# Performance work log

Measured on AMD Instinct MI355X. Metric: run time of the kernel, lower is better.

## Reference

```python
import jax, jax.numpy as jnp
import numpy as np

E = 256      # embedding_dim
H = 16       # head_num
D = 16       # qkv_dim
FF = 512     # ff_hidden_dim
L = 5        # encoder_layer_num
B = 4        # batch
N = 256      # node_cnt
EPS = 1e-5   # InstanceNorm eps


def setup_inputs() -> dict:
    key = jax.random.key(0)
    ks = jax.random.split(key, 16)
    s = 0.05

    def nrm(k, shape):
        return jax.random.normal(k, shape, dtype=jnp.float32) * s

    return {
        "data": jax.random.normal(ks[0], (B, N, N), dtype=jnp.float32),
        "node_rand": jax.random.uniform(ks[1], (B, N, 1), dtype=jnp.float32),
        # Cross_Encoder input projections (Linear(1, E))
        "Wnode": nrm(ks[2], (1, E)), "bnode": jnp.zeros((E,), jnp.float32),
        "Wedge": nrm(ks[3], (1, E)), "bedge": jnp.zeros((E,), jnp.float32),
        # Per layer (L) x per block (2: row/col) weights
        "Wq": nrm(ks[4], (L, 2, E, H * D)),
        "Wk": nrm(ks[5], (L, 2, E, H * D)),
        "Wv": nrm(ks[6], (L, 2, E, H * D)),
        "Wcomb": nrm(ks[7], (L, 2, H * D, E)),
        "bcomb": jnp.zeros((L, 2, E), jnp.float32),
        "n1w": jnp.ones((L, 2, E), jnp.float32),
        "n1b": jnp.zeros((L, 2, E), jnp.float32),
        "W1": nrm(ks[8], (L, 2, E, FF)),
        "b1": jnp.zeros((L, 2, FF), jnp.float32),
        "W2": nrm(ks[9], (L, 2, FF, E)),
        "b2": jnp.zeros((L, 2, E), jnp.float32),
        "n2w": jnp.ones((L, 2, E), jnp.float32),
        "n2b": jnp.zeros((L, 2, E), jnp.float32),
        # MixedScore edge-bias projection per block: E -> H channels
        "Wmix": nrm(ks[10], (L, 2, E, H)),
    }


def _instance_norm(x, w, b):
    # x: [B, N, E]; InstanceNorm1d after transpose -> normalize over node dim N per (B, channel)
    mu = jnp.mean(x, axis=1, keepdims=True)
    var = jnp.var(x, axis=1, keepdims=True)
    return (x - mu) * jax.lax.rsqrt(var + EPS) * w + b


def reference(data, node_rand, Wnode, bnode, Wedge, bedge,
              Wq, Wk, Wv, Wcomb, bcomb, n1w, n1b,
              W1, b1, W2, b2, n2w, n2b, Wmix):
    inv_sqrt_d = jnp.float32(1.0) / jnp.sqrt(jnp.float32(D))

    def block(row, col, edge, i, j):
        # row, col: [B, N, E]; edge: [B, N, N, E]
        q = (row @ Wq[i, j]).reshape(B, N, H, D)
        k = (col @ Wk[i, j]).reshape(B, N, H, D)
        v = (col @ Wv[i, j]).reshape(B, N, H, D)
        score = jnp.einsum('bnhd,bmhd->bhnm', q, k) * inv_sqrt_d
        score = score + jnp.einsum('bnme,eh->bhnm', edge, Wmix[i, j])
        w = jax.nn.softmax(score, axis=-1)
        out = jnp.einsum('bhnm,bmhd->bnhd', w, v).reshape(B, N, H * D)
        mh = out @ Wcomb[i, j] + bcomb[i, j]
        o1 = _instance_norm(row + mh, n1w[i, j], n1b[i, j])
        ff = jax.nn.relu(o1 @ W1[i, j] + b1[i, j]) @ W2[i, j] + b2[i, j]
        return _instance_norm(o1 + ff, n2w[i, j], n2b[i, j])

    # compute_normalized_matrices: per-batch global min-max scaling
    flat = data.reshape(B, -1)
    mn = flat.min(axis=1).reshape(B, 1, 1)
    mx = flat.max(axis=1).reshape(B, 1, 1)
    rng = mx - mn
    rng = jnp.where(rng == 0, jnp.float32(1.0), rng)
    scaled = (data - mn) / rng

    edge = scaled[..., None] @ Wedge + bedge           # [B, N, N, E]
    emb = node_rand @ Wnode + bnode                    # [B, N, E]

    row, col = emb, emb
    for i in range(L):
        row_new = block(row, col, edge, i, 0)
        col = block(col, row, jnp.swapaxes(edge, 1, 2), i, 1)
        row = row_new
    return row, col
```

## Files before the change

kernel.cpp:

```cpp
#include <hip/hip_runtime.h>
#include <hip/hip_bf16.h>

#define E 256
#define H 16
#define DD 16
#define FFH 512
#define LAYERS 5
#define BB 4
#define NN 256
#define MROWS 1024

typedef __attribute__((ext_vector_type(8))) short bfrag;
typedef __attribute__((ext_vector_type(4))) float f32x4;
typedef __attribute__((ext_vector_type(8))) unsigned short us8;
typedef unsigned short u16;

__device__ __forceinline__ void bsplit(float v, u16& h, u16& l) {
    unsigned u = __float_as_uint(v);
    u16 hh = (u16)((u + 0x7fffu + ((u >> 16) & 1u)) >> 16);
    float r = v - __uint_as_float((unsigned)hh << 16);
    unsigned u2 = __float_as_uint(r);
    h = hh;
    l = (u16)((u2 + 0x7fffu + ((u2 >> 16) & 1u)) >> 16);
}

union PrepS {
    float tile[32 * 33];
    struct { u16 th[64 * 40], tl[64 * 40]; } wp;
    struct { float smin[4], smax[4]; } mm;
};

__global__ __launch_bounds__(256) void k_prep(
    const float* __restrict__ data, const float* __restrict__ node_rand,
    const float* __restrict__ Wnode, const float* __restrict__ bnode,
    const float* __restrict__ Wedge, const float* __restrict__ bedge,
    const float* __restrict__ Wmix,
    const float* __restrict__ Wq, const float* __restrict__ Wk, const float* __restrict__ Wv,
    const float* __restrict__ Wc, const float* __restrict__ W1, const float* __restrict__ W2,
    float* __restrict__ pmin, float* __restrict__ pmax, float* __restrict__ c1c0,
    float* __restrict__ rowb, float* __restrict__ colb,
    u16* rowh, u16* rowl, u16* colh, u16* coll,
    float* __restrict__ dataT,
    u16* qh, u16* ql, u16* kh, u16* kl_, u16* vh, u16* vl,
    u16* ch, u16* cl, u16* f1h, u16* f1l, u16* f2h, u16* f2l) {
    __shared__ PrepS ps;
    int bid = blockIdx.x;
    int t = threadIdx.x;
    if (bid < 64) {
        int b = bid >> 4, p = bid & 15;
        const float* src = data + (size_t)b * NN * NN + p * 4096;
        float lmin = 1e30f, lmax = -1e30f;
        #pragma unroll
        for (int i = 0; i < 16; i++) {
            float v = src[t + i * 256];
            lmin = fminf(lmin, v);
            lmax = fmaxf(lmax, v);
        }
        #pragma unroll
        for (int off = 32; off; off >>= 1) {
            lmin = fminf(lmin, __shfl_down(lmin, off));
            lmax = fmaxf(lmax, __shfl_down(lmax, off));
        }
        int wid = t >> 6, lane = t & 63;
        if (lane == 0) { ps.mm.smin[wid] = lmin; ps.mm.smax[wid] = lmax; }
        __syncthreads();
        if (t == 0) {
            pmin[b * 16 + p] = fminf(fminf(ps.mm.smin[0], ps.mm.smin[1]), fminf(ps.mm.smin[2], ps.mm.smin[3]));
            pmax[b * 16 + p] = fmaxf(fmaxf(ps.mm.smax[0], ps.mm.smax[1]), fmaxf(ps.mm.smax[2], ps.mm.smax[3]));
        }
    } else if (bid < 1088) {
        int idx = (bid - 64) * 256 + t;
        int bn = idx >> 8, e = idx & 255;
        float v = node_rand[bn] * Wnode[e] + bnode[e];
        rowb[idx] = v;
        colb[idx] = v;
        u16 h, l;
        bsplit(v, h, l);
        rowh[idx] = h; rowl[idx] = l;
        colh[idx] = h; coll[idx] = l;
    } else if (bid < 1344) {
        int local = bid - 1088;
        int bx = local & 7, by = (local >> 3) & 7, b = local >> 6;
        int r0 = by * 32, c0 = bx * 32;
        int tx = t & 31, ty = t >> 5;
        const float* src = data + (size_t)b * NN * NN;
        float* dst = dataT + (size_t)b * NN * NN;
        #pragma unroll
        for (int i = 0; i < 4; i++)
            ps.tile[(ty + 8 * i) * 33 + tx] = src[(size_t)(r0 + ty + 8 * i) * NN + c0 + tx];
        __syncthreads();
        #pragma unroll
        for (int i = 0; i < 4; i++)
            dst[(size_t)(c0 + ty + 8 * i) * NN + r0 + tx] = ps.tile[tx * 33 + ty + 8 * i];
    } else if (bid < 3904) {
        int id = bid - 1344;
        const float* W; u16 *Dh, *Dl; int K, N, mat, s, nt;
        if (id < 1280) {
            int seg = id / 320, local = id % 320;
            mat = local >> 5; int rem = local & 31; s = rem >> 2; nt = rem & 3;
            K = 256; N = 256;
            W  = seg == 0 ? Wq : seg == 1 ? Wk : seg == 2 ? Wv : Wc;
            Dh = seg == 0 ? qh : seg == 1 ? kh : seg == 2 ? vh : ch;
            Dl = seg == 0 ? ql : seg == 1 ? kl_ : seg == 2 ? vl : cl;
        } else if (id < 1920) {
            int local = id - 1280;
            mat = local >> 6; int rem = local & 63; s = rem >> 3; nt = rem & 7;
            K = 256; N = 512; W = W1; Dh = f1h; Dl = f1l;
        } else {
            int local = id - 1920;
            mat = local >> 6; int rem = local & 63; s = rem >> 2; nt = rem & 3;
            K = 512; N = 256; W = W2; Dh = f2h; Dl = f2l;
        }
        int kk = t >> 3, nl = (t & 7) * 8;
        const float* p = W + (size_t)mat * K * N + (size_t)(s * 32 + kk) * N + nt * 64 + nl;
        float4 f0 = *(const float4*)p;
        float4 f1v = *(const float4*)(p + 4);
        float fv[8] = {f0.x, f0.y, f0.z, f0.w, f1v.x, f1v.y, f1v.z, f1v.w};
        #pragma unroll
        for (int i = 0; i < 8; i++) bsplit(fv[i], ps.wp.th[(nl + i) * 40 + kk], ps.wp.tl[(nl + i) * 40 + kk]);
        __syncthreads();
        int n = t >> 2, ko = (t & 3) * 8;
        size_t dbase = (size_t)mat * K * N + (size_t)s * N * 32 + (size_t)nt * 64 * 32
                     + (size_t)n * 32 + ko;
        *(us8*)(Dh + dbase) = *(const us8*)&ps.wp.th[n * 40 + ko];
        *(us8*)(Dl + dbase) = *(const us8*)&ps.wp.tl[n * 40 + ko];
    } else {
        if (t < LAYERS * 2 * H) {
            int lj = t >> 4, h = t & 15;
            float c1 = 0.f, c0 = 0.f;
            for (int e = 0; e < E; e++) {
                float wm = Wmix[(lj * E + e) * H + h];
                c1 += Wedge[e] * wm;
                c0 += bedge[e] * wm;
            }
            c1c0[t] = c1;
            c1c0[160 + t] = c0;
        }
    }
}

__device__ __forceinline__ void mfma_gemm(const u16* __restrict__ Ah, const u16* __restrict__ Al,
                                          const u16* __restrict__ Bh, const u16* __restrict__ Bl,
                                          const float* __restrict__ bias, const float* __restrict__ R,
                                          float* __restrict__ Cf, u16* __restrict__ Ch,
                                          u16* __restrict__ Cl, int K, int Ncols, int relu) {
    __shared__ u16 AsH[32 * 136], AsL[32 * 136], BsH[64 * 136], BsL[64 * 136];
    int t = threadIdx.x;
    int lane = t & 63, wave = t >> 6;
    int quad = lane >> 4, l16 = lane & 15;
    int wy = wave >> 1, wx = wave & 1;
    int mBase = blockIdx.x * 32, nBase = blockIdx.y * 64;
    f32x4 acc0 = {0.f, 0.f, 0.f, 0.f}, acc1 = acc0;
    int arow = t >> 3, ak = (t & 7) * 16;
    int bcol = lane, bq = wave;
    const int nslab = K >> 7;
    const u16* apH = Ah + (size_t)(mBase + arow) * K + ak;
    const u16* apL = Al + (size_t)(mBase + arow) * K + ak;
    const size_t sstr = (size_t)Ncols * 32;
    size_t bbase = (size_t)bq * sstr + (size_t)(nBase + bcol) * 32;
    const u16* bpH = Bh + bbase;
    const u16* bpL = Bl + bbase;
    us8 rah0 = *(const us8*)apH, rah1 = *(const us8*)(apH + 8);
    us8 ral0 = *(const us8*)apL, ral1 = *(const us8*)(apL + 8);
    us8 rbh0 = *(const us8*)(bpH + 0);
    us8 rbh1 = *(const us8*)(bpH + 8);
    us8 rbh2 = *(const us8*)(bpH + 16);
    us8 rbh3 = *(const us8*)(bpH + 24);
    us8 rbl0 = *(const us8*)(bpL + 0);
    us8 rbl1 = *(const us8*)(bpL + 8);
    us8 rbl2 = *(const us8*)(bpL + 16);
    us8 rbl3 = *(const us8*)(bpL + 24);
    for (int s = 0; s < nslab; s++) {
        __syncthreads();
        *(us8*)&AsH[arow * 136 + ak] = rah0;  *(us8*)&AsH[arow * 136 + ak + 8] = rah1;
        *(us8*)&AsL[arow * 136 + ak] = ral0;  *(us8*)&AsL[arow * 136 + ak + 8] = ral1;
        {
            int bb = bcol * 136 + bq * 32;
            *(us8*)&BsH[bb + 0] = rbh0;  *(us8*)&BsH[bb + 8] = rbh1;
            *(us8*)&BsH[bb + 16] = rbh2; *(us8*)&BsH[bb + 24] = rbh3;
            *(us8*)&BsL[bb + 0] = rbl0;  *(us8*)&BsL[bb + 8] = rbl1;
            *(us8*)&BsL[bb + 16] = rbl2; *(us8*)&BsL[bb + 24] = rbl3;
        }
        __syncthreads();
        if (s + 1 < nslab) {
            rah0 = *(const us8*)(apH + (s + 1) * 128);
            rah1 = *(const us8*)(apH + (s + 1) * 128 + 8);
            ral0 = *(const us8*)(apL + (s + 1) * 128);
            ral1 = *(const us8*)(apL + (s + 1) * 128 + 8);
            const u16* nbH = bpH + (size_t)(4 * (s + 1)) * sstr;
            const u16* nbL = bpL + (size_t)(4 * (s + 1)) * sstr;
            rbh0 = *(const us8*)(nbH + 0);  rbh1 = *(const us8*)(nbH + 8);
            rbh2 = *(const us8*)(nbH + 16); rbh3 = *(const us8*)(nbH + 24);
            rbl0 = *(const us8*)(nbL + 0);  rbl1 = *(const us8*)(nbL + 8);
            rbl2 = *(const us8*)(nbL + 16); rbl3 = *(const us8*)(nbL + 24);
        }
        #pragma unroll
        for (int c = 0; c < 4; c++) {
            bfrag a_h = *(const bfrag*)&AsH[(wy * 16 + l16) * 136 + c * 32 + quad * 8];
            bfrag a_l = *(const bfrag*)&AsL[(wy * 16 + l16) * 136 + c * 32 + quad * 8];
            bfrag b_h0 = *(const bfrag*)&BsH[(wx * 32 + l16) * 136 + c * 32 + quad * 8];
            bfrag b_h1 = *(const bfrag*)&BsH[(wx * 32 + 16 + l16) * 136 + c * 32 + quad * 8];
            bfrag b_l0 = *(const bfrag*)&BsL[(wx * 32 + l16) * 136 + c * 32 + quad * 8];
            bfrag b_l1 = *(const bfrag*)&BsL[(wx * 32 + 16 + l16) * 136 + c * 32 + quad * 8];
            acc0 = __builtin_amdgcn_mfma_f32_16x16x32_bf16(a_h, b_h0, acc0, 0, 0, 0);
            acc1 = __builtin_amdgcn_mfma_f32_16x16x32_bf16(a_h, b_h1, acc1, 0, 0, 0);
            acc0 = __builtin_amdgcn_mfma_f32_16x16x32_bf16(a_h, b_l0, acc0, 0, 0, 0);
            acc1 = __builtin_amdgcn_mfma_f32_16x16x32_bf16(a_h, b_l1, acc1, 0, 0, 0);
            acc0 = __builtin_amdgcn_mfma_f32_16x16x32_bf16(a_l, b_h0, acc0, 0, 0, 0);
            acc1 = __builtin_amdgcn_mfma_f32_16x16x32_bf16(a_l, b_h1, acc1, 0, 0, 0);
        }
    }
    int col0 = nBase + wx * 32 + l16;
    int col1 = col0 + 16;
    float bia0 = bias ? bias[col0] : 0.f;
    float bia1 = bias ? bias[col1] : 0.f;
    #pragma unroll
    for (int r = 0; r < 4; r++) {
        int row0 = mBase + wy * 16 + quad * 4 + r;
        float v0 = acc0[r] + bia0, v1 = acc1[r] + bia1;
        if (R) {
            v0 += R[(size_t)row0 * Ncols + col0];
            v1 += R[(size_t)row0 * Ncols + col1];
        }
        if (relu) {
            v0 = fmaxf(v0, 0.f); v1 = fmaxf(v1, 0.f);
        }
        if (Cf) {
            Cf[(size_t)row0 * Ncols + col0] = v0;
            Cf[(size_t)row0 * Ncols + col1] = v1;
        } else {
            u16 h, l;
            bsplit(v0, h, l); Ch[(size_t)row0 * Ncols + col0] = h; Cl[(size_t)row0 * Ncols + col0] = l;
            bsplit(v1, h, l); Ch[(size_t)row0 * Ncols + col1] = h; Cl[(size_t)row0 * Ncols + col1] = l;
        }
    }
}

__global__ __launch_bounds__(256) void k_qkv(const u16* __restrict__ rowh, const u16* __restrict__ rowl,
                                             const u16* __restrict__ colh, const u16* __restrict__ coll,
                                             const u16* __restrict__ WqTh, const u16* __restrict__ WqTl,
                                             const u16* __restrict__ WkTh, const u16* __restrict__ WkTl,
                                             const u16* __restrict__ WvTh, const u16* __restrict__ WvTl,
                                             int lb2,
                                             float* q0, float* k0, float* v0,
                                             float* q1, float* k1, float* v1) {
    int z = blockIdx.z;
    int j = z / 3, w = z % 3;
    const u16* Ah = (w == 0) ? (j ? colh : rowh) : (j ? rowh : colh);
    const u16* Al = (w == 0) ? (j ? coll : rowl) : (j ? rowl : coll);
    const u16* Wh = (w == 0 ? WqTh : (w == 1 ? WkTh : WvTh)) + (size_t)(lb2 + j) * E * E;
    const u16* Wl = (w == 0 ? WqTl : (w == 1 ? WkTl : WvTl)) + (size_t)(lb2 + j) * E * E;
    float* outs[6] = {q0, k0, v0, q1, k1, v1};
    mfma_gemm(Ah, Al, Wh, Wl, nullptr, nullptr, outs[z], nullptr, nullptr, E, E, 0);
}

__global__ __launch_bounds__(256) void k_mgemm(const u16* Ah0, const u16* Al0,
                                               const u16* Ah1, const u16* Al1,
                                               const u16* __restrict__ Bh, const u16* __restrict__ Bl,
                                               int lb2, long wstride,
                                               const float* __restrict__ biasl, int bstride,
                                               const float* R0, const float* R1,
                                               float* Cf0, float* Cf1,
                                               u16* Ch0, u16* Cl0, u16* Ch1, u16* Cl1,
                                               int K, int Ncols, int relu) {
    int j = blockIdx.z;
    mfma_gemm(j ? Ah1 : Ah0, j ? Al1 : Al0,
              Bh + (size_t)(lb2 + j) * wstride, Bl + (size_t)(lb2 + j) * wstride,
              biasl ? biasl + (size_t)j * bstride : nullptr,
              R0 ? (j ? R1 : R0) : nullptr,
              Cf0 ? (j ? Cf1 : Cf0) : nullptr,
              Ch0 ? (j ? Ch1 : Ch0) : nullptr,
              Cl0 ? (j ? Cl1 : Cl0) : nullptr,
              K, Ncols, relu);
}

__global__ __launch_bounds__(256) void k_attn(const float* __restrict__ q0, const float* __restrict__ k0,
                                              const float* __restrict__ v0, const float* __restrict__ q1,
                                              const float* __restrict__ k1, const float* __restrict__ v1,
                                              const float* __restrict__ data, const float* __restrict__ dataT,
                                              const float* __restrict__ pmin, const float* __restrict__ pmax,
                                              const float* __restrict__ c1c0, int lj_base,
                                              u16* __restrict__ atth0, u16* __restrict__ attl0,
                                              u16* __restrict__ atth1, u16* __restrict__ attl1) {
    int wgid = blockIdx.x;
    int r8 = wgid & 7;
    int qd = wgid >> 3;
    int ng = qd & 7;
    int bhj = r8 * 16 + (qd >> 3);
    int bh = bhj >> 1;
    int j = bhj & 1;
    int b = bh >> 4, h = bh & 15;
    const float* q = j ? q1 : q0;
    const float* k = j ? k1 : k0;
    const float* v = j ? v1 : v0;
    float mn = 1e30f, mx = -1e30f;
    #pragma unroll
    for (int p = 0; p < 16; p++) {
        mn = fminf(mn, pmin[b * 16 + p]);
        mx = fmaxf(mx, pmax[b * 16 + p]);
    }
    float rng = mx - mn;
    if (rng == 0.f) rng = 1.f;
    float inv = 1.f / rng;
    float c1 = c1c0[(lj_base + j) * 16 + h];
    float c0 = c1c0[160 + (lj_base + j) * 16 + h];
    float c1p = inv * c1;
    float c0p = c0 - mn * c1p;

    __shared__ float kl[256 * 20];
    __shared__ float vl[256 * 20];
    int t = threadIdx.x;
    int lane = t & 63, w = t >> 6;
    int r = lane >> 3, ml = lane & 7;
    int n = ng * 32 + w * 8 + r;

    float qr[16];
    const float* qp = q + ((size_t)(b * NN + n) * E) + h * DD;
    #pragma unroll
    for (int d4 = 0; d4 < 4; d4++) {
        float4 q4 = *(const float4*)(qp + d4 * 4);
        qr[d4 * 4 + 0] = q4.x; qr[d4 * 4 + 1] = q4.y;
        qr[d4 * 4 + 2] = q4.z; qr[d4 * 4 + 3] = q4.w;
    }

    {
        int c = t & 3, mb = t >> 2;
        #pragma unroll
        for (int it = 0; it < 4; it++) {
            int m = mb + 64 * it;
            const float* kp = k + ((size_t)(b * NN + m) * E) + h * DD + c * 4;
            const float* vp = v + ((size_t)(b * NN + m) * E) + h * DD + c * 4;
            *(float4*)&kl[m * 20 + c * 4] = *(const float4*)kp;
            *(float4*)&vl[m * 20 + c * 4] = *(const float4*)vp;
        }
    }
    __syncthreads();

    const float* pedge = (j ? dataT : data) + (size_t)b * NN * NN + (size_t)n * NN;

    float sum = 0.f;
    float acc[16] = {};
    for (int i = 0; i < 32; i++) {
        int m = ml + 8 * i;
        float4 ka = *(const float4*)&kl[m * 20 + 0];
        float4 kb = *(const float4*)&kl[m * 20 + 4];
        float4 kc = *(const float4*)&kl[m * 20 + 8];
        float4 kd = *(const float4*)&kl[m * 20 + 12];
        float s0 = qr[0] * ka.x + qr[1] * ka.y + qr[2] * ka.z + qr[3] * ka.w;
        float s1 = qr[4] * kb.x + qr[5] * kb.y + qr[6] * kb.z + qr[7] * kb.w;
        float s2 = qr[8] * kc.x + qr[9] * kc.y + qr[10] * kc.z + qr[11] * kc.w;
        float s3 = qr[12] * kd.x + qr[13] * kd.y + qr[14] * kd.z + qr[15] * kd.w;
        float s = ((s0 + s1) + (s2 + s3)) * 0.25f + pedge[m] * c1p + c0p;
        float e = __expf(s);
        sum += e;
        float4 va = *(const float4*)&vl[m * 20 + 0];
        float4 vb = *(const float4*)&vl[m * 20 + 4];
        float4 vc = *(const float4*)&vl[m * 20 + 8];
        float4 vd = *(const float4*)&vl[m * 20 + 12];
        acc[0] += e * va.x;  acc[1] += e * va.y;  acc[2] += e * va.z;  acc[3] += e * va.w;
        acc[4] += e * vb.x;  acc[5] += e * vb.y;  acc[6] += e * vb.z;  acc[7] += e * vb.w;
        acc[8] += e * vc.x;  acc[9] += e * vc.y;  acc[10] += e * vc.z; acc[11] += e * vc.w;
        acc[12] += e * vd.x; acc[13] += e * vd.y; acc[14] += e * vd.z; acc[15] += e * vd.w;
    }
    #pragma unroll
    for (int mask = 1; mask <= 4; mask <<= 1) {
        sum += __shfl_xor(sum, mask);
        #pragma unroll
        for (int d = 0; d < 16; d++) acc[d] += __shfl_xor(acc[d], mask);
    }
    if (ml == 0) {
        float invs = 1.f / sum;
        u16 hh[16], ll[16];
        #pragma unroll
        for (int d = 0; d < 16; d++) bsplit(acc[d] * invs, hh[d], ll[d]);
        size_t base = ((size_t)(b * NN + n) * E) + h * DD;
        u16* oh = (j ? atth1 : atth0) + base;
        u16* ol = (j ? attl1 : attl0) + base;
        *(us8*)oh = *(const us8*)&hh[0];
        *(us8*)(oh + 8) = *(const us8*)&hh[8];
        *(us8*)ol = *(const us8*)&ll[0];
        *(us8*)(ol + 8) = *(const us8*)&ll[8];
    }
}

__global__ __launch_bounds__(256) void k_inorm(const float* __restrict__ Y0, const float* __restrict__ Y1,
                                               const float* __restrict__ wl, const float* __restrict__ bl,
                                               int pstride,
                                               float* Of0, float* Of1,
                                               u16* Oh0, u16* Ol0, u16* Oh1, u16* Ol1,
                                               float* __restrict__ fout) {
    int b = blockIdx.x, j = blockIdx.y;
    int ec = blockIdx.z * 8;
    const float* Y = (j ? Y1 : Y0) + (size_t)b * NN * E;
    float* O = (j ? Of1 : Of0) + (size_t)b * NN * E;
    u16* Oh = (j ? Oh1 : Oh0) + (size_t)b * NN * E;
    u16* Ol = (j ? Ol1 : Ol0) + (size_t)b * NN * E;
    const float* w = wl + (size_t)j * pstride;
    const float* bb = bl + (size_t)j * pstride;
    int t = threadIdx.x;
    int et = t & 7, n0 = t >> 3;
    int e = ec + et;
    float vals[8];
    float s = 0.f, s2 = 0.f;
    #pragma unroll
    for (int kk = 0; kk < 8; kk++) {
        float v = Y[(size_t)(n0 + 32 * kk) * E + e];
        vals[kk] = v;
        s += v;
        s2 += v * v;
    }
    __shared__ float ps[32 * 9], ps2[32 * 9];
    ps[n0 * 9 + et] = s;
    ps2[n0 * 9 + et] = s2;
    __syncthreads();
    float st = 0.f, st2 = 0.f;
    #pragma unroll
    for (int kk = 0; kk < 32; kk++) { st += ps[kk * 9 + et]; st2 += ps2[kk * 9 + et]; }
    float mu = st * (1.f / NN);
    float var = fmaxf(st2 * (1.f / NN) - mu * mu, 0.f);
    float scale = w[e] * rsqrtf(var + 1e-5f);
    float shift = bb[e] - mu * scale;
    #pragma unroll
    for (int kk = 0; kk < 8; kk++) {
        float vv = vals[kk] * scale + shift;
        size_t idx = (size_t)(n0 + 32 * kk) * E + e;
        O[idx] = vv;
        u16 hh, ll;
        bsplit(vv, hh, ll);
        Oh[idx] = hh;
        Ol[idx] = ll;
        if (fout) fout[(size_t)j * (BB * NN * E) + (size_t)b * NN * E + idx] = vv;
    }
}


extern "C" void kernel_launch(void* const* d_in, const int* in_sizes, int n_in,
                              void* d_out, int out_size, void* d_ws, size_t ws_size,
                              hipStream_t stream) {
    const float* data      = (const float*)d_in[0];
    const float* node_rand = (const float*)d_in[1];
    const float* Wnode     = (const float*)d_in[2];
    const float* bnode     = (const float*)d_in[3];
    const float* Wedge     = (const float*)d_in[4];
    const float* bedge     = (const float*)d_in[5];
    const float* Wq        = (const float*)d_in[6];
    const float* Wk        = (const float*)d_in[7];
    const float* Wv        = (const float*)d_in[8];
    const float* Wcomb     = (const float*)d_in[9];
    const float* bcomb     = (const float*)d_in[10];
    const float* n1w       = (const float*)d_in[11];
    const float* n1b       = (const float*)d_in[12];
    const float* W1        = (const float*)d_in[13];
    const float* b1        = (const float*)d_in[14];
    const float* W2        = (const float*)d_in[15];
    const float* b2        = (const float*)d_in[16];
    const float* n2w       = (const float*)d_in[17];
    const float* n2b       = (const float*)d_in[18];
    const float* Wmix      = (const float*)d_in[19];
    float* out = (float*)d_out;

    float* ws = (float*)d_ws;
    const size_t T = (size_t)MROWS * E;
    const size_t TF = (size_t)MROWS * FFH;
    float* dataT = ws + 0 * T;
    float* row   = ws + 1 * T;
    float* col   = ws + 2 * T;
    float* q0    = ws + 3 * T;
    float* q1    = ws + 4 * T;
    float* k0    = ws + 5 * T;
    float* k1    = ws + 6 * T;
    float* v0    = ws + 7 * T;
    float* v1    = ws + 8 * T;
    float* o1f0  = ws + 9 * T;
    float* o1f1  = ws + 10 * T;
    float* pmin  = ws + 11 * T;
    float* pmax  = pmin + 64;
    float* c1c0  = pmax + 64;
    u16* us = (u16*)(ws + 11 * T + 512);
    auto nxt = [&](size_t n) { u16* p = us; us += n; return p; };
    u16* rowh = nxt(T);  u16* rowl = nxt(T);
    u16* colh = nxt(T);  u16* coll = nxt(T);
    u16* atth0 = nxt(T); u16* attl0 = nxt(T);
    u16* atth1 = nxt(T); u16* attl1 = nxt(T);
    u16* o1h0 = nxt(T);  u16* o1l0 = nxt(T);
    u16* o1h1 = nxt(T);  u16* o1l1 = nxt(T);
    u16* ffhh0 = nxt(TF); u16* ffhl0 = nxt(TF);
    u16* ffhh1 = nxt(TF); u16* ffhl1 = nxt(TF);
    const size_t EE10 = (size_t)10 * E * E;
    const size_t EF10 = (size_t)10 * E * FFH;
    u16* WqTh = nxt(EE10); u16* WqTl = nxt(EE10);
    u16* WkTh = nxt(EE10); u16* WkTl = nxt(EE10);
    u16* WvTh = nxt(EE10); u16* WvTl = nxt(EE10);
    u16* WcTh = nxt(EE10); u16* WcTl = nxt(EE10);
    u16* W1Th = nxt(EF10); u16* W1Tl = nxt(EF10);
    u16* W2Th = nxt(EF10); u16* W2Tl = nxt(EF10);
    float* y0 = q0;   float* y1 = q1;
    float* y20 = q0;  float* y21 = q1;

    k_prep<<<3905, 256, 0, stream>>>(data, node_rand, Wnode, bnode,
                                     Wedge, bedge, Wmix,
                                     Wq, Wk, Wv, Wcomb, W1, W2,
                                     pmin, pmax, c1c0,
                                     row, col, rowh, rowl, colh, coll, dataT,
                                     WqTh, WqTl, WkTh, WkTl, WvTh, WvTl,
                                     WcTh, WcTl, W1Th, W1Tl, W2Th, W2Tl);

    for (int l = 0; l < LAYERS; l++) {
        int lb2 = l * 2;
        k_qkv<<<dim3(32, 4, 6), 256, 0, stream>>>(rowh, rowl, colh, coll,
                                                  WqTh, WqTl, WkTh, WkTl, WvTh, WvTl, lb2,
                                                  q0, k0, v0, q1, k1, v1);
        k_attn<<<dim3(1024), 256, 0, stream>>>(q0, k0, v0, q1, k1, v1, data, dataT,
                                               pmin, pmax, c1c0, lb2,
                                               atth0, attl0, atth1, attl1);
        k_mgemm<<<dim3(32, 4, 2), 256, 0, stream>>>(atth0, attl0, atth1, attl1,
                                                    WcTh, WcTl, lb2, (long)E * E,
                                                    bcomb, E,
                                                    row, col, y0, y1,
                                                    nullptr, nullptr, nullptr, nullptr,
                                                    E, E, 0);
        k_inorm<<<dim3(BB, 2, 32), 256, 0, stream>>>(y0, y1,
                                                     n1w + (size_t)lb2 * E, n1b + (size_t)lb2 * E, E,
                                                     o1f0, o1f1, o1h0, o1l0, o1h1, o1l1, nullptr);
        k_mgemm<<<dim3(32, 8, 2), 256, 0, stream>>>(o1h0, o1l0, o1h1, o1l1,
                                                    W1Th, W1Tl, lb2, (long)E * FFH,
                                                    b1, FFH,
                                                    nullptr, nullptr, nullptr, nullptr,
                                                    ffhh0, ffhl0, ffhh1, ffhl1,
                                                    E, FFH, 1);
        k_mgemm<<<dim3(32, 4, 2), 256, 0, stream>>>(ffhh0, ffhl0, ffhh1, ffhl1,
                                                    W2Th, W2Tl, lb2, (long)FFH * E,
                                                    b2, E,
                                                    o1f0, o1f1, q0 , q1 ,
                                                    nullptr, nullptr, nullptr, nullptr,
                                                    FFH, E, 0);
        k_inorm<<<dim3(BB, 2, 32), 256, 0, stream>>>(y20, y21,
                                                     n2w + (size_t)lb2 * E, n2b + (size_t)lb2 * E, E,
                                                     row, col, rowh, rowl, colh, coll,
                                                     (l == LAYERS - 1) ? out : nullptr);
    }
}
```

Before: 406.8 us.

## Split attention head dim across lanes and halve K/V LDS tile

The attention kernel now splits each query's 16-wide head dimension across two lanes, combining partial dot products with a cross-lane shuffle. Each block covers 16 query rows instead of 32, so the grid doubles. K/V are staged into LDS in two 128-row phases to halve shared memory, and launch bounds request 8 blocks per CU. The goal is fewer registers, less LDS and higher occupancy, paid for with an extra shuffle per key, an extra barrier, and K/V reloaded by twice as many blocks.

```diff
diff --git a/kernel.cpp b/kernel.cpp
--- a/kernel.cpp
+++ b/kernel.cpp
@@ -274,19 +274,19 @@
               K, Ncols, relu);
 }
 
-__global__ __launch_bounds__(256) void k_attn(const float* __restrict__ q0, const float* __restrict__ k0,
-                                              const float* __restrict__ v0, const float* __restrict__ q1,
-                                              const float* __restrict__ k1, const float* __restrict__ v1,
-                                              const float* __restrict__ data, const float* __restrict__ dataT,
-                                              const float* __restrict__ pmin, const float* __restrict__ pmax,
-                                              const float* __restrict__ c1c0, int lj_base,
-                                              u16* __restrict__ atth0, u16* __restrict__ attl0,
-                                              u16* __restrict__ atth1, u16* __restrict__ attl1) {
+__global__ __launch_bounds__(256, 8) void k_attn(const float* __restrict__ q0, const float* __restrict__ k0,
+                                                 const float* __restrict__ v0, const float* __restrict__ q1,
+                                                 const float* __restrict__ k1, const float* __restrict__ v1,
+                                                 const float* __restrict__ data, const float* __restrict__ dataT,
+                                                 const float* __restrict__ pmin, const float* __restrict__ pmax,
+                                                 const float* __restrict__ c1c0, int lj_base,
+                                                 u16* __restrict__ atth0, u16* __restrict__ attl0,
+                                                 u16* __restrict__ atth1, u16* __restrict__ attl1) {
     int wgid = blockIdx.x;
     int r8 = wgid & 7;
     int qd = wgid >> 3;
-    int ng = qd & 7;
-    int bhj = r8 * 16 + (qd >> 3);
+    int ng = qd & 15;
+    int bhj = r8 * 16 + (qd >> 4);
     int bh = bhj >> 1;
     int j = bhj & 1;
     int b = bh >> 4, h = bh & 15;
@@ -302,84 +302,76 @@
     float rng = mx - mn;
     if (rng == 0.f) rng = 1.f;
     float inv = 1.f / rng;
-    float c1 = c1c0[(lj_base + j) * 16 + h];
-    float c0 = c1c0[160 + (lj_base + j) * 16 + h];
-    float c1p = inv * c1;
-    float c0p = c0 - mn * c1p;
-
-    __shared__ float kl[256 * 20];
-    __shared__ float vl[256 * 20];
+    float c1p = inv * c1c0[(lj_base + j) * 16 + h];
+    float c0p = c1c0[160 + (lj_base + j) * 16 + h] - mn * c1p;
+
+    __shared__ float kl[128 * 20];
+    __shared__ float vl[128 * 20];
     int t = threadIdx.x;
     int lane = t & 63, w = t >> 6;
-    int r = lane >> 3, ml = lane & 7;
-    int n = ng * 32 + w * 8 + r;
-
-    float qr[16];
-    const float* qp = q + ((size_t)(b * NN + n) * E) + h * DD;
-    #pragma unroll
-    for (int d4 = 0; d4 < 4; d4++) {
-        float4 q4 = *(const float4*)(qp + d4 * 4);
-        qr[d4 * 4 + 0] = q4.x; qr[d4 * 4 + 1] = q4.y;
-        qr[d4 * 4 + 2] = q4.z; qr[d4 * 4 + 3] = q4.w;
-    }
-
+    int nq = lane >> 4;
+    int dh = (lane >> 3) & 1;
+    int ml = lane & 7;
+    int n = ng * 16 + w * 4 + nq;
+
+    float qr[8];
     {
-        int c = t & 3, mb = t >> 2;
-        #pragma unroll
-        for (int it = 0; it < 4; it++) {
-            int m = mb + 64 * it;
-            const float* kp = k + ((size_t)(b * NN + m) * E) + h * DD + c * 4;
-            const float* vp = v + ((size_t)(b * NN + m) * E) + h * DD + c * 4;
-            *(float4*)&kl[m * 20 + c * 4] = *(const float4*)kp;
-            *(float4*)&vl[m * 20 + c * 4] = *(const float4*)vp;
-        }
-    }
-    __syncthreads();
-
+        const float* qp = q + ((size_t)(b * NN + n) * E) + h * DD + dh * 8;
+        float4 qa = *(const float4*)qp;
+        float4 qb = *(const float4*)(qp + 4);
+        qr[0] = qa.x; qr[1] = qa.y; qr[2] = qa.z; qr[3] = qa.w;
+        qr[4] = qb.x; qr[5] = qb.y; qr[6] = qb.z; qr[7] = qb.w;
+    }
     const float* pedge = (j ? dataT : data) + (size_t)b * NN * NN + (size_t)n * NN;
 
     float sum = 0.f;
-    float acc[16] = {};
-    for (int i = 0; i < 32; i++) {
-        int m = ml + 8 * i;
-        float4 ka = *(const float4*)&kl[m * 20 + 0];
-        float4 kb = *(const float4*)&kl[m * 20 + 4];
-        float4 kc = *(const float4*)&kl[m * 20 + 8];
-        float4 kd = *(const float4*)&kl[m * 20 + 12];
-        float s0 = qr[0] * ka.x + qr[1] * ka.y + qr[2] * ka.z + qr[3] * ka.w;
-        float s1 = qr[4] * kb.x + qr[5] * kb.y + qr[6] * kb.z + qr[7] * kb.w;
-        float s2 = qr[8] * kc.x + qr[9] * kc.y + qr[10] * kc.z + qr[11] * kc.w;
-        float s3 = qr[12] * kd.x + qr[13] * kd.y + qr[14] * kd.z + qr[15] * kd.w;
-        float s = ((s0 + s1) + (s2 + s3)) * 0.25f + pedge[m] * c1p + c0p;
-        float e = __expf(s);
-        sum += e;
-        float4 va = *(const float4*)&vl[m * 20 + 0];
-        float4 vb = *(const float4*)&vl[m * 20 + 4];
-        float4 vc = *(const float4*)&vl[m * 20 + 8];
-        float4 vd = *(const float4*)&vl[m * 20 + 12];
-        acc[0] += e * va.x;  acc[1] += e * va.y;  acc[2] += e * va.z;  acc[3] += e * va.w;
-        acc[4] += e * vb.x;  acc[5] += e * vb.y;  acc[6] += e * vb.z;  acc[7] += e * vb.w;
-        acc[8] += e * vc.x;  acc[9] += e * vc.y;  acc[10] += e * vc.z; acc[11] += e * vc.w;
-        acc[12] += e * vd.x; acc[13] += e * vd.y; acc[14] += e * vd.z; acc[15] += e * vd.w;
+    float acc[8] = {};
+    int sc = t & 3, sr = t >> 2;
+    for (int ph = 0; ph < 2; ph++) {
+        if (ph) __syncthreads();
+        #pragma unroll
+        for (int it = 0; it < 2; it++) {
+            int rl = sr + 64 * it;
+            int mrow = ph * 128 + rl;
+            const float* kp = k + ((size_t)(b * NN + mrow) * E) + h * DD + sc * 4;
+            const float* vp = v + ((size_t)(b * NN + mrow) * E) + h * DD + sc * 4;
+            *(float4*)&kl[rl * 20 + sc * 4] = *(const float4*)kp;
+            *(float4*)&vl[rl * 20 + sc * 4] = *(const float4*)vp;
+        }
+        __syncthreads();
+        #pragma unroll 4
+        for (int i = 0; i < 16; i++) {
+            int m = 8 * i + ml;
+            float4 ka = *(const float4*)&kl[m * 20 + dh * 8];
+            float4 kb = *(const float4*)&kl[m * 20 + dh * 8 + 4];
+            float sA = (qr[0] * ka.x + qr[1] * ka.y + qr[2] * ka.z + qr[3] * ka.w)
+                     + (qr[4] * kb.x + qr[5] * kb.y + qr[6] * kb.z + qr[7] * kb.w);
+            float sB = __shfl_xor(sA, 8);
+            float s = (sA + sB) * 0.25f + pedge[ph * 128 + m] * c1p + c0p;
+            float e = __expf(s);
+            sum += e;
+            float4 va = *(const float4*)&vl[m * 20 + dh * 8];
+            float4 vb = *(const float4*)&vl[m * 20 + dh * 8 + 4];
+            acc[0] += e * va.x; acc[1] += e * va.y; acc[2] += e * va.z; acc[3] += e * va.w;
+            acc[4] += e * vb.x; acc[5] += e * vb.y; acc[6] += e * vb.z; acc[7] += e * vb.w;
+        }
     }
     #pragma unroll
     for (int mask = 1; mask <= 4; mask <<= 1) {
         sum += __shfl_xor(sum, mask);
         #pragma unroll
-        for (int d = 0; d < 16; d++) acc[d] += __shfl_xor(acc[d], mask);
+        for (int d = 0; d < 8; d++) acc[d] += __shfl_xor(acc[d], mask);
     }
     if (ml == 0) {
         float invs = 1.f / sum;
-        u16 hh[16], ll[16];
-        #pragma unroll
-        for (int d = 0; d < 16; d++) bsplit(acc[d] * invs, hh[d], ll[d]);
-        size_t base = ((size_t)(b * NN + n) * E) + h * DD;
+        u16 hh[8], ll[8];
+        #pragma unroll
+        for (int d = 0; d < 8; d++) bsplit(acc[d] * invs, hh[d], ll[d]);
+        size_t base = ((size_t)(b * NN + n) * E) + h * DD + dh * 8;
         u16* oh = (j ? atth1 : atth0) + base;
         u16* ol = (j ? attl1 : attl0) + base;
         *(us8*)oh = *(const us8*)&hh[0];
-        *(us8*)(oh + 8) = *(const us8*)&hh[8];
         *(us8*)ol = *(const us8*)&ll[0];
-        *(us8*)(ol + 8) = *(const us8*)&ll[8];
     }
 }
 
@@ -510,7 +502,7 @@
         k_qkv<<<dim3(32, 4, 6), 256, 0, stream>>>(rowh, rowl, colh, coll,
                                                   WqTh, WqTl, WkTh, WkTl, WvTh, WvTl, lb2,
                                                   q0, k0, v0, q1, k1, v1);
-        k_attn<<<dim3(1024), 256, 0, stream>>>(q0, k0, v0, q1, k1, v1, data, dataT,
+        k_attn<<<dim3(2048), 256, 0, stream>>>(q0, k0, v0, q1, k1, v1, data, dataT,
                                                pmin, pmax, c1c0, lb2,
                                                atth0, attl0, atth1, attl1);
         k_mgemm<<<dim3(32, 4, 2), 256, 0, stream>>>(atth0, attl0, atth1, attl1,
```

Result: slower. 441.2 us (+8.5%).
